# Kernel tuning notes

Hardware: AMD Instinct MI355X
Metric: run time of the kernel (lower is better)

Reference implementation:

```python
import jax, jax.numpy as jnp
import numpy as np

C = 201        # n_classes + 1 (background)
K = 5          # prototypes per class
DIM = 768
B = 64
HP = 16        # patch grid side, n_patches = HP*HP
N_PATCH = HP * HP
GAMMA = 0.999
SK_ITERS = 3
EPS = 1e-12


def setup_inputs() -> dict:
    key = jax.random.key(0)
    k1, k2, k3, k4 = jax.random.split(key, 4)
    return dict(
        patch_tokens=jax.random.normal(k1, (B, N_PATCH, DIM), jnp.float32),
        prototypes=jax.random.normal(k2, (C, K, DIM), jnp.float32) * 0.02,  # trunc_normal(std=0.02) approx
        sa=jnp.full((C - 1, K), 0.5, jnp.float32),                          # sa_init=0.5
        scale=jnp.float32(4.0),                                             # scale_init=4.0
        labels=jax.random.randint(k3, (B,), 0, C - 1),                      # image-level labels in [0, 200)
        masks=jax.random.bernoulli(k4, 0.5, (B, HP, HP)),                   # fg_extractor output
    )


def _masked_sinkhorn(L, m, n_iters=SK_ITERS):
    """Sinkhorn-Knopp over a masked subset of rows.
    L: [N, K] logits, m: [N] bool row mask. Rows outside m stay zero.
    Equivalent to running SK on the gathered rows L[m] (softmax init,
    alternating column/row normalization)."""
    Q = jax.nn.softmax(L, axis=-1) * m[:, None]

    def body(Q, _):
        Q = Q / (Q.sum(axis=0, keepdims=True) + EPS)                         # column normalize
        Q = jnp.where(m[:, None], Q / (Q.sum(axis=1, keepdims=True) + EPS), 0.0)  # row normalize (masked rows)
        return Q, None

    Q, _ = jax.lax.scan(body, Q, None, length=n_iters)
    return Q


def reference(patch_tokens, prototypes, sa, scale, labels, masks):
    # --- cosine patch-prototype logits ---
    tok = patch_tokens / (jnp.linalg.norm(patch_tokens, axis=-1, keepdims=True) + EPS)
    pro = prototypes / (jnp.linalg.norm(prototypes, axis=-1, keepdims=True) + EPS)
    patch_prototype_logits = jnp.einsum('bnd,ckd->bnck', tok, pro)           # [B, N, C, K]

    # --- avg pooling over patches ---
    image_prototype_logits = patch_prototype_logits.mean(axis=1)             # [B, C, K]

    # --- 'sa' classification head ---
    sa_w = jax.nn.softmax(sa, axis=-1) * K                                   # [C-1, K]
    class_logits = (scale * image_prototype_logits[:, :-1, :] * sa_w).sum(-1)  # [B, C-1]

    # --- pseudo patch labels from fg masks ---
    pseudo_patch_labels = jnp.where(masks, labels[:, None, None], C - 1)     # [B, H, W] int
    pl_flat = pseudo_patch_labels.reshape(-1)                                # [B*N]

    # --- online clustering (operates on detached values in the original) ---
    tok_flat = jax.lax.stop_gradient(tok).reshape(-1, DIM)                   # [B*N, D]
    L_flat = jax.lax.stop_gradient(patch_prototype_logits).reshape(-1, C, K)  # [B*N, C, K]
    class_mask = pl_flat[None, :] == jnp.arange(C)[:, None]                  # [C, B*N]

    # vectorized per-class masked Sinkhorn-Knopp (replaces dynamic python loop over unique labels)
    Q_all = jax.vmap(_masked_sinkhorn, in_axes=(1, 0))(L_flat, class_mask)   # [C, B*N, K]

    # prototype candidates: P_c_new = L_c_assignment^T @ I_c (masked rows are zero)
    P_new_c = jnp.einsum('cnk,nd->ckd', Q_all, tok_flat)                     # [C, K, D]
    has_class = class_mask.any(axis=1)[:, None, None]
    new_prototypes = jnp.where(has_class,
                               GAMMA * prototypes + (1.0 - GAMMA) * P_new_c,
                               prototypes)

    # part assignment: argmax over K, gathered at each patch's own class
    idx_all = jnp.argmax(Q_all, axis=-1)                                     # [C, B*N]
    part_assignment_maps = idx_all[pl_flat, jnp.arange(pl_flat.shape[0])].reshape(B, N_PATCH)

    return (patch_prototype_logits, image_prototype_logits, class_logits,
            part_assignment_maps, new_prototypes, pseudo_patch_labels)
```

## Files before the change

### kernel.cpp

```cpp
#include <hip/hip_runtime.h>
#include <hip/hip_cooperative_groups.h>
#include <math.h>

namespace cg = cooperative_groups;

#define NTOK 16384
#define NPRO 1005
#define DIMD 768
#define CKD  1005
#define CC   201
#define KKp  5
#define BGC  200
#define KEXP 2304
#define KA   1536
#define NPAD 1024

#define OUT_LOGITS   0
#define OUT_IMG      16465920
#define OUT_CLS      (OUT_IMG + 64320)
#define OUT_PART     (OUT_CLS + 12800)
#define OUT_NEWPROTO (OUT_PART + 16384)
#define OUT_PSEUDO   (OUT_NEWPROTO + 771840)

#define WOFF_PACC    0ULL
#define WOFF_COLSUM3 3087360ULL
#define WOFF_COUNTS  3099648ULL
#define WOFF_FLAG    3100672ULL
#define WS_ZERO_B    3100928ULL
#define WOFF_A2      3100928ULL
#define WOFF_B2      53432576ULL
#define WOFF_INVTOK  58151168ULL
#define WOFF_PL      58216704ULL
#define WOFF_Q       58282240ULL
#define WOFF_OFFSETS 58609920ULL
#define WOFF_CURSORS 58610944ULL
#define WOFF_ORDER   58611968ULL

typedef __attribute__((ext_vector_type(8))) short short8;
typedef __attribute__((ext_vector_type(4))) float f32x4;
typedef __attribute__((ext_vector_type(4))) unsigned short usv4;

__device__ __forceinline__ unsigned short f2bf(float x) {
  unsigned int b = __float_as_uint(x);
  unsigned int r = (b + 0x7FFFu + ((b >> 16) & 1u)) >> 16;
  return (unsigned short)r;
}
__device__ __forceinline__ float bf2f(unsigned short u) {
  return __uint_as_float(((unsigned int)u) << 16);
}

__device__ __forceinline__ void async_copy16(const void* g, void* lds) {
  __builtin_amdgcn_global_load_lds(
      (const __attribute__((address_space(1))) unsigned int*)g,
      (__attribute__((address_space(3))) unsigned int*)lds, 16, 0, 0);
}

__global__ __launch_bounds__(256) void conv_kernel(const float* __restrict__ tok,
                                                   const float* __restrict__ pro,
                                                   unsigned short* __restrict__ A2,
                                                   unsigned short* __restrict__ B2,
                                                   float* __restrict__ inv_tok) {
  int wid = (blockIdx.x * 256 + threadIdx.x) >> 6;
  int lane = threadIdx.x & 63;
  if (wid >= NTOK + NPAD) return;

  if (wid < NTOK) {
    const float4* s4 = (const float4*)(tok + (size_t)wid * DIMD);
    float4 v[3];
    float s = 0.0f;
#pragma unroll
    for (int p = 0; p < 3; ++p) {
      v[p] = s4[p * 64 + lane];
      s += v[p].x * v[p].x + v[p].y * v[p].y + v[p].z * v[p].z + v[p].w * v[p].w;
    }
#pragma unroll
    for (int off = 32; off; off >>= 1) s += __shfl_xor(s, off, 64);
    float inv = 1.0f / (sqrtf(s) + 1e-12f);
    if (lane == 0) inv_tok[wid] = inv;
    unsigned short* rowp = A2 + (size_t)wid * KA;
#pragma unroll
    for (int p = 0; p < 3; ++p) {
      float x0 = v[p].x * inv, x1 = v[p].y * inv, x2 = v[p].z * inv, x3 = v[p].w * inv;
      usv4 hi, lo;
      hi.x = f2bf(x0); hi.y = f2bf(x1); hi.z = f2bf(x2); hi.w = f2bf(x3);
      lo.x = f2bf(x0 - bf2f(hi.x)); lo.y = f2bf(x1 - bf2f(hi.y));
      lo.z = f2bf(x2 - bf2f(hi.z)); lo.w = f2bf(x3 - bf2f(hi.w));
      int c = p * 256 + lane * 4;
      *(usv4*)(rowp + c) = hi;
      *(usv4*)(rowp + 768 + c) = lo;
    }
  } else {
    int pw = wid - NTOK;
    unsigned short* rowp = B2 + (size_t)pw * KEXP;
    if (pw >= NPRO) {
      usv4 z = {0, 0, 0, 0};
#pragma unroll
      for (int p = 0; p < 3; ++p) {
        int c = p * 256 + lane * 4;
        *(usv4*)(rowp + c) = z; *(usv4*)(rowp + 768 + c) = z; *(usv4*)(rowp + 1536 + c) = z;
      }
      return;
    }
    const float4* s4 = (const float4*)(pro + (size_t)pw * DIMD);
    float4 v[3];
    float s = 0.0f;
#pragma unroll
    for (int p = 0; p < 3; ++p) {
      v[p] = s4[p * 64 + lane];
      s += v[p].x * v[p].x + v[p].y * v[p].y + v[p].z * v[p].z + v[p].w * v[p].w;
    }
#pragma unroll
    for (int off = 32; off; off >>= 1) s += __shfl_xor(s, off, 64);
    float inv = 1.0f / (sqrtf(s) + 1e-12f);
#pragma unroll
    for (int p = 0; p < 3; ++p) {
      float x0 = v[p].x * inv, x1 = v[p].y * inv, x2 = v[p].z * inv, x3 = v[p].w * inv;
      usv4 hi, lo;
      hi.x = f2bf(x0); hi.y = f2bf(x1); hi.z = f2bf(x2); hi.w = f2bf(x3);
      lo.x = f2bf(x0 - bf2f(hi.x)); lo.y = f2bf(x1 - bf2f(hi.y));
      lo.z = f2bf(x2 - bf2f(hi.z)); lo.w = f2bf(x3 - bf2f(hi.w));
      int c = p * 256 + lane * 4;
      *(usv4*)(rowp + c) = hi;
      *(usv4*)(rowp + 768 + c) = hi;
      *(usv4*)(rowp + 1536 + c) = lo;
    }
  }
}

__global__ __launch_bounds__(256, 2) void gemm_kernel(const unsigned short* __restrict__ A2,
                                                      const unsigned short* __restrict__ B2,
                                                      float* __restrict__ C,
                                                      float* __restrict__ img) {
  __shared__ unsigned short As[2][4096];
  __shared__ unsigned short Bs[2][4096];
  const int tid = threadIdx.x;
  const int lane = tid & 63, wave = tid >> 6;
  const int m0 = blockIdx.x * 128, n0 = blockIdx.y * 128;
  const int wr = wave >> 1, wc = wave & 1;

  f32x4 acc[4][4];
#pragma unroll
  for (int i = 0; i < 4; ++i)
#pragma unroll
    for (int j = 0; j < 4; ++j) acc[i][j] = (f32x4){0.f, 0.f, 0.f, 0.f};

  const int r4 = lane >> 2;
  const int kc = (lane & 3) * 8;

  auto STAGE = [&](int buf, int kt) {
    int kb = kt * 32;
    int acol = (kb < KA ? kb : kb - KA) + kc;
    int bcol = kb + kc;
#pragma unroll
    for (int j = 0; j < 2; ++j) {
      int seg = wave * 2 + j;
      async_copy16(A2 + (size_t)(m0 + seg * 16 + r4) * KA + acol, &As[buf][seg * 512]);
      async_copy16(B2 + (size_t)(n0 + seg * 16 + r4) * KEXP + bcol, &Bs[buf][seg * 512]);
    }
  };

  STAGE(0, 0);
  __syncthreads();

  const int rb = wr * 64 + (lane & 15);
  const int cb = wc * 64 + (lane & 15);
  const int hi8 = (lane >> 4) * 8;

  int cur = 0;
  for (int kt = 0; kt < 72; ++kt) {
    if (kt < 71) STAGE(cur ^ 1, kt + 1);
    short8 a[4], b[4];
#pragma unroll
    for (int ff = 0; ff < 4; ++ff) {
      a[ff] = *(const short8*)&As[cur][(rb + ff * 16) * 32 + hi8];
      b[ff] = *(const short8*)&Bs[cur][(cb + ff * 16) * 32 + hi8];
    }
#pragma unroll
    for (int fm = 0; fm < 4; ++fm)
#pragma unroll
      for (int fn = 0; fn < 4; ++fn)
        acc[fm][fn] = __builtin_amdgcn_mfma_f32_16x16x32_bf16(a[fm], b[fn], acc[fm][fn], 0, 0, 0);
    __syncthreads();
    cur ^= 1;
  }

  const int bimg = m0 >> 8;
#pragma unroll
  for (int fn = 0; fn < 4; ++fn) {
    int col = n0 + wc * 64 + fn * 16 + (lane & 15);
    float s = 0.0f;
#pragma unroll
    for (int fm = 0; fm < 4; ++fm) {
      int row = m0 + wr * 64 + fm * 16 + (lane >> 4) * 4;
      f32x4 v = acc[fm][fn];
      if (col < NPRO) {
        C[(size_t)(row + 0) * CKD + col] = v.x;
        C[(size_t)(row + 1) * CKD + col] = v.y;
        C[(size_t)(row + 2) * CKD + col] = v.z;
        C[(size_t)(row + 3) * CKD + col] = v.w;
      }
      s += v.x + v.y + v.z + v.w;
    }
    s += __shfl_xor(s, 16, 64);
    s += __shfl_xor(s, 32, 64);
    if (lane < 16 && col < NPRO)
      atomicAdd(&img[bimg * CKD + col], s * (1.0f / 256.0f));
  }
}

__global__ __launch_bounds__(256) void cls_kernel(const float* __restrict__ img,
                                                  const float* __restrict__ sa,
                                                  const float* __restrict__ scale,
                                                  float* __restrict__ out_cls) {
  int gid = blockIdx.x * 256 + threadIdx.x;
  if (gid >= 64 * 200) return;
  int b = gid / 200, c = gid - b * 200;
  float s5[KKp];
  float mx = -1e30f;
#pragma unroll
  for (int k = 0; k < KKp; ++k) { s5[k] = sa[c * KKp + k]; mx = fmaxf(mx, s5[k]); }
  float den = 0.0f;
#pragma unroll
  for (int k = 0; k < KKp; ++k) { s5[k] = expf(s5[k] - mx); den += s5[k]; }
  float acc = 0.0f;
#pragma unroll
  for (int k = 0; k < KKp; ++k)
    acc += img[(size_t)b * CKD + c * KKp + k] * (s5[k] / den * 5.0f);
  out_cls[gid] = scale[0] * acc;
}

__global__ __launch_bounds__(256) void cluster_kernel(const void* __restrict__ masks,
                                                      const int* __restrict__ labels,
                                                      const float* __restrict__ L,
                                                      float* __restrict__ Q,
                                                      int* __restrict__ pl,
                                                      float* __restrict__ out_pseudo,
                                                      float* __restrict__ out_part,
                                                      int* __restrict__ counts,
                                                      int* __restrict__ offsets,
                                                      int* __restrict__ cursors,
                                                      int* __restrict__ order,
                                                      float* __restrict__ colsum3,
                                                      int* __restrict__ flag) {
  cg::grid_group g = cg::this_grid();
  const int b = blockIdx.x, t = threadIdx.x;
  const int n = b * 256 + t;
  const int lane = t & 63, w = t >> 6;

  __shared__ int wcnt[4];
  __shared__ int sbase[2];
  __shared__ float red[4][2 * KKp];
  __shared__ int sc[256];

  if (t < 64) {
    unsigned v = ((const unsigned*)masks)[b * 64 + t];
    unsigned pr = (v == 0x3F800000u) ? 1u : (v > 1u ? 2u : 0u);
    if (pr) atomicOr(flag, (int)pr);
  }
  g.sync();
  int f = __hip_atomic_load(flag, __ATOMIC_RELAXED, __HIP_MEMORY_SCOPE_AGENT);

  int m;
  if (f & 1)      m = ((const float*)masks)[n] != 0.0f;
  else if (f & 2) m = ((const unsigned char*)masks)[n] != 0;
  else            m = ((const int*)masks)[n] != 0;
  const int cf = labels[b];
  const int lab = m ? cf : BGC;
  pl[n] = lab;
  out_pseudo[n] = (float)lab;

  unsigned long long mk = __ballot(m != 0);
  int rkw_fg = __popcll(mk & ((1ull << lane) - 1));
  int rkw_bg = lane - rkw_fg;
  if (lane == 0) wcnt[w] = __popcll(mk);
  __syncthreads();
  int fg_before = 0;
#pragma unroll
  for (int i = 0; i < 4; ++i) fg_before += (i < w) ? wcnt[i] : 0;
  int nf = wcnt[0] + wcnt[1] + wcnt[2] + wcnt[3];
  int fgrank = fg_before + rkw_fg;
  int bgrank = (w * 64 - fg_before) + rkw_bg;
  if (t == 0) {
    atomicAdd(&counts[cf], nf);
    atomicAdd(&counts[BGC], 256 - nf);
  }

  const float* Lr = L + (size_t)n * CKD + lab * KKp;
  float q[KKp];
  float mx = -1e30f;
#pragma unroll
  for (int k = 0; k < KKp; ++k) { q[k] = Lr[k]; mx = fmaxf(mx, q[k]); }
  float den = 0.0f;
#pragma unroll
  for (int k = 0; k < KKp; ++k) { q[k] = expf(q[k] - mx); den += q[k]; }
  float inv = 1.0f / den;
#pragma unroll
  for (int k = 0; k < KKp; ++k) q[k] *= inv;

  for (int it = 0; it < 3; ++it) {
    float fgv[KKp], bgv[KKp];
#pragma unroll
    for (int k = 0; k < KKp; ++k) { fgv[k] = m ? q[k] : 0.0f; bgv[k] = m ? 0.0f : q[k]; }
#pragma unroll
    for (int off = 32; off; off >>= 1) {
#pragma unroll
      for (int k = 0; k < KKp; ++k) {
        fgv[k] += __shfl_xor(fgv[k], off, 64);
        bgv[k] += __shfl_xor(bgv[k], off, 64);
      }
    }
    if (lane == 0) {
#pragma unroll
      for (int k = 0; k < KKp; ++k) { red[w][k] = fgv[k]; red[w][KKp + k] = bgv[k]; }
    }
    __syncthreads();
    if (t < 2 * KKp) {
      float s = red[0][t] + red[1][t] + red[2][t] + red[3][t];
      int cls_ = (t < KKp) ? cf : BGC;
      int kk = (t < KKp) ? t : t - KKp;
      atomicAdd(&colsum3[it * 1024 + cls_ * KKp + kk], s);
    }
    g.sync();

    if (it == 0 && b == 0) {
      int v0 = (t < CC) ? counts[t] : 0;
      sc[t] = v0;
      __syncthreads();
      for (int off = 1; off < 256; off <<= 1) {
        int u = (t >= off) ? sc[t - off] : 0;
        __syncthreads();
        sc[t] += u;
        __syncthreads();
      }
      if (t < CC) { offsets[t] = sc[t] - v0; cursors[t] = sc[t] - v0; }
      if (t == CC - 1) offsets[CC] = sc[t];
    }

    float r = 0.0f;
#pragma unroll
    for (int k = 0; k < KKp; ++k) {
      q[k] = q[k] / (colsum3[it * 1024 + lab * KKp + k] + 1e-12f);
      r += q[k];
    }
    float rinv = 1.0f / (r + 1e-12f);
#pragma unroll
    for (int k = 0; k < KKp; ++k) q[k] *= rinv;
  }

  float* Qr = Q + (size_t)n * KKp;
  float best = q[0];
  int bi = 0;
#pragma unroll
  for (int k = 0; k < KKp; ++k) {
    Qr[k] = q[k];
    if (k > 0 && q[k] > best) { best = q[k]; bi = k; }
  }
  out_part[n] = (float)bi;

  if (t == 0) {
    sbase[0] = atomicAdd(&cursors[cf], nf);
    sbase[1] = atomicAdd(&cursors[BGC], 256 - nf);
  }
  __syncthreads();
  int base = m ? sbase[0] : sbase[1];
  int rank = m ? fgrank : bgrank;
  order[base + rank] = n;
}

__global__ __launch_bounds__(256) void pnew_kernel(const int* __restrict__ order,
                                                   const int* __restrict__ pl,
                                                   const float* __restrict__ Q,
                                                   const float* __restrict__ tok,
                                                   const float* __restrict__ inv_tok,
                                                   float* __restrict__ P_acc) {
  __shared__ int idx[32], cls[32];
  int t = threadIdx.x;
  int p0 = blockIdx.x * 32;
  if (t < 32) {
    int n = order[p0 + t];
    idx[t] = n;
    cls[t] = pl[n];
  }
  __syncthreads();
  float acc[KKp][3];
#pragma unroll
  for (int k = 0; k < KKp; ++k)
#pragma unroll
    for (int s = 0; s < 3; ++s) acc[k][s] = 0.0f;
  int cur = cls[0];
  for (int i = 0; i < 32; ++i) {
    int c = cls[i];
    if (c != cur) {
#pragma unroll
      for (int k = 0; k < KKp; ++k)
#pragma unroll
        for (int s = 0; s < 3; ++s) {
          atomicAdd(&P_acc[((size_t)cur * KKp + k) * DIMD + s * 256 + t], acc[k][s]);
          acc[k][s] = 0.0f;
        }
      cur = c;
    }
    int n = idx[i];
    float it = inv_tok[n];
    float q[KKp];
#pragma unroll
    for (int k = 0; k < KKp; ++k) q[k] = Q[(size_t)n * KKp + k];
#pragma unroll
    for (int s = 0; s < 3; ++s) {
      float v = tok[(size_t)n * DIMD + s * 256 + t] * it;
#pragma unroll
      for (int k = 0; k < KKp; ++k) acc[k][s] = fmaf(q[k], v, acc[k][s]);
    }
  }
#pragma unroll
  for (int k = 0; k < KKp; ++k)
#pragma unroll
    for (int s = 0; s < 3; ++s)
      atomicAdd(&P_acc[((size_t)cur * KKp + k) * DIMD + s * 256 + t], acc[k][s]);
}

__global__ __launch_bounds__(256) void newproto_kernel(const float* __restrict__ proto,
                                                       const float* __restrict__ P_acc,
                                                       const int* __restrict__ offsets,
                                                       float* __restrict__ outp) {
  int gid = blockIdx.x * 256 + threadIdx.x;
  if (gid >= CC * KKp * DIMD) return;
  int c = gid / (KKp * DIMD);
  float p = proto[gid];
  bool has = offsets[c + 1] > offsets[c];
  outp[gid] = has ? (0.999f * p + 0.001f * P_acc[gid]) : p;
}

extern "C" void kernel_launch(void* const* d_in, const int* in_sizes, int n_in,
                              void* d_out, int out_size, void* d_ws, size_t ws_size,
                              hipStream_t stream) {
  const float* patch_tokens = (const float*)d_in[0];
  const float* prototypes   = (const float*)d_in[1];
  const float* sa           = (const float*)d_in[2];
  const float* scale        = (const float*)d_in[3];
  const int*   labels       = (const int*)d_in[4];
  const void*  masks        = (const void*)d_in[5];

  float* out = (float*)d_out;
  float* out_logits  = out + OUT_LOGITS;
  float* out_img     = out + OUT_IMG;
  float* out_cls     = out + OUT_CLS;
  float* out_part    = out + OUT_PART;
  float* out_newp    = out + OUT_NEWPROTO;
  float* out_pseudo  = out + OUT_PSEUDO;

  char* w = (char*)d_ws;
  float*          P_acc   = (float*)(w + WOFF_PACC);
  float*          colsum3 = (float*)(w + WOFF_COLSUM3);
  int*            counts  = (int*)(w + WOFF_COUNTS);
  int*            flag    = (int*)(w + WOFF_FLAG);
  unsigned short* A2      = (unsigned short*)(w + WOFF_A2);
  unsigned short* B2      = (unsigned short*)(w + WOFF_B2);
  float*          inv_tok = (float*)(w + WOFF_INVTOK);
  int*            pl      = (int*)(w + WOFF_PL);
  float*          Q       = (float*)(w + WOFF_Q);
  int*            offsets = (int*)(w + WOFF_OFFSETS);
  int*            cursors = (int*)(w + WOFF_CURSORS);
  int*            order   = (int*)(w + WOFF_ORDER);

  hipMemsetAsync(d_ws, 0, WS_ZERO_B, stream);
  hipMemsetAsync(out_img, 0, (size_t)64 * CKD * sizeof(float), stream);

  conv_kernel<<<4352, 256, 0, stream>>>(patch_tokens, prototypes, A2, B2, inv_tok);

  gemm_kernel<<<dim3(128, 8), 256, 0, stream>>>(A2, B2, out_logits, out_img);

  cls_kernel<<<50, 256, 0, stream>>>(out_img, sa, scale, out_cls);

  {
    const void* masks_a = masks; const int* labels_a = labels;
    const float* L_a = out_logits; float* Q_a = Q;
    int* pl_a = pl; float* pseudo_a = out_pseudo; float* part_a = out_part;
    int* counts_a = counts; int* offsets_a = offsets; int* cursors_a = cursors;
    int* order_a = order; float* colsum3_a = colsum3; int* flag_a = flag;
    void* cargs[] = {&masks_a, &labels_a, &L_a, &Q_a, &pl_a, &pseudo_a, &part_a,
                     &counts_a, &offsets_a, &cursors_a, &order_a, &colsum3_a, &flag_a};
    hipLaunchCooperativeKernel((const void*)cluster_kernel, dim3(64), dim3(256),
                               cargs, 0, stream);
  }

  pnew_kernel<<<512, 256, 0, stream>>>(order, pl, Q, patch_tokens, inv_tok, P_acc);
  newproto_kernel<<<3015, 256, 0, stream>>>(prototypes, P_acc, offsets, out_newp);
}
```

Before: 321.1 us.

## Enlarge GEMM tile to 256x256 with swizzled LDS pipeline; fold cls into cluster

The logits GEMM goes from a 128x128 tile with 4 waves to a 256x256 tile with 8 waves. It uses 128KB of dynamic LDS with a swizzled layout, K-steps of 64, and staged half-tile async loads interleaved with MFMA phases using barriers and setprio. The goal is more data reuse per block and less LDS bank conflict and global traffic. The separate cls_kernel is merged into the cooperative cluster_kernel, which removes one launch. The trade-off is higher register pressure and far fewer blocks (256 instead of 1024), which may hurt occupancy and load balance.

```diff
diff --git a/kernel.cpp b/kernel.cpp
--- a/kernel.cpp
+++ b/kernel.cpp
@@ -14,6 +14,7 @@
 #define KEXP 2304
 #define KA   1536
 #define NPAD 1024
+#define NT   36
 
 #define OUT_LOGITS   0
 #define OUT_IMG      16465920
@@ -127,71 +128,143 @@
   }
 }
 
-__global__ __launch_bounds__(256, 2) void gemm_kernel(const unsigned short* __restrict__ A2,
+__global__ __launch_bounds__(512, 2) void gemm_kernel(const unsigned short* __restrict__ A2,
                                                       const unsigned short* __restrict__ B2,
                                                       float* __restrict__ C,
                                                       float* __restrict__ img) {
-  __shared__ unsigned short As[2][4096];
-  __shared__ unsigned short Bs[2][4096];
+  extern __shared__ unsigned char lds[];
   const int tid = threadIdx.x;
-  const int lane = tid & 63, wave = tid >> 6;
-  const int m0 = blockIdx.x * 128, n0 = blockIdx.y * 128;
-  const int wr = wave >> 1, wc = wave & 1;
-
-  f32x4 acc[4][4];
-#pragma unroll
-  for (int i = 0; i < 4; ++i)
+  const int l = tid & 63, w = tid >> 6;
+  const int wr = w >> 2, wn = w & 3;
+  const int m0 = blockIdx.x * 256, n0 = blockIdx.y * 256;
+
+  f32x4 acc[8][4];
+#pragma unroll
+  for (int i = 0; i < 8; ++i)
 #pragma unroll
     for (int j = 0; j < 4; ++j) acc[i][j] = (f32x4){0.f, 0.f, 0.f, 0.f};
 
-  const int r4 = lane >> 2;
-  const int kc = (lane & 3) * 8;
-
-  auto STAGE = [&](int buf, int kt) {
-    int kb = kt * 32;
-    int acol = (kb < KA ? kb : kb - KA) + kc;
-    int bcol = kb + kc;
+  auto STAGE = [&](int t, int isB, int half) {
+    const int buf = t & 1;
+    unsigned char* dst = lds + (isB ? 65536 : 0) + buf * 32768 + half * 16384 + w * 1024;
+    const char* gsrc;
+    int rs;
+    if (isB) {
+      gsrc = (const char*)B2 + (size_t)(n0 + half * 128) * 4608 + (size_t)t * 128;
+      rs = 4608;
+    } else {
+      int ac = (t < 24 ? t : t - 24) * 128;
+      gsrc = (const char*)A2 + (size_t)(m0 + half * 128) * 3072 + ac;
+      rs = 3072;
+    }
 #pragma unroll
     for (int j = 0; j < 2; ++j) {
-      int seg = wave * 2 + j;
-      async_copy16(A2 + (size_t)(m0 + seg * 16 + r4) * KA + acol, &As[buf][seg * 512]);
-      async_copy16(B2 + (size_t)(n0 + seg * 16 + r4) * KEXP + bcol, &Bs[buf][seg * 512]);
+      int X = j * 8192 + w * 1024 + l * 16;
+      int P = X ^ (((X >> 8) & 1) << 4) ^ (((X >> 9) & 1) << 5);
+      int row = P >> 7, colb = P & 127;
+      async_copy16(gsrc + (size_t)row * rs + colb, dst + j * 8192);
     }
   };
 
-  STAGE(0, 0);
-  __syncthreads();
-
-  const int rb = wr * 64 + (lane & 15);
-  const int cb = wc * 64 + (lane & 15);
-  const int hi8 = (lane >> 4) * 8;
-
-  int cur = 0;
-  for (int kt = 0; kt < 72; ++kt) {
-    if (kt < 71) STAGE(cur ^ 1, kt + 1);
-    short8 a[4], b[4];
-#pragma unroll
-    for (int ff = 0; ff < 4; ++ff) {
-      a[ff] = *(const short8*)&As[cur][(rb + ff * 16) * 32 + hi8];
-      b[ff] = *(const short8*)&Bs[cur][(cb + ff * 16) * 32 + hi8];
-    }
+  STAGE(0, 0, 0); STAGE(0, 0, 1); STAGE(0, 1, 0); STAGE(0, 1, 1);
+  STAGE(1, 0, 0); STAGE(1, 0, 1);
+  asm volatile("s_waitcnt vmcnt(4)" ::: "memory");
+  __builtin_amdgcn_s_barrier();
+
+  const int lx = ((l >> 4) * 16) ^ ((l & 6) << 3);
+  const int arow = (l & 15) * 128 + lx;
+
+  short8 a0[4][2], a1[4][2], b0[2][2], b1[2][2];
+
+#pragma unroll 1
+  for (int t = 0; t < NT; ++t) {
+    const int buf = t & 1;
+    const unsigned char* ab = lds + buf * 32768 + wr * 16384;
+    const unsigned char* bb = lds + 65536 + buf * 32768 + (wn >> 1) * 16384 + (wn & 1) * 8192;
+
 #pragma unroll
     for (int fm = 0; fm < 4; ++fm)
 #pragma unroll
-      for (int fn = 0; fn < 4; ++fn)
-        acc[fm][fn] = __builtin_amdgcn_mfma_f32_16x16x32_bf16(a[fm], b[fn], acc[fm][fn], 0, 0, 0);
-    __syncthreads();
-    cur ^= 1;
+      for (int ks = 0; ks < 2; ++ks)
+        a0[fm][ks] = *(const short8*)(ab + fm * 2048 + ks * 64 + arow);
+#pragma unroll
+    for (int fn = 0; fn < 2; ++fn)
+#pragma unroll
+      for (int ks = 0; ks < 2; ++ks)
+        b0[fn][ks] = *(const short8*)(bb + fn * 2048 + ks * 64 + arow);
+    if (t + 1 < NT) STAGE(t + 1, 1, 0);
+    __builtin_amdgcn_s_barrier();
+    __builtin_amdgcn_s_setprio(1);
+#pragma unroll
+    for (int fm = 0; fm < 4; ++fm)
+#pragma unroll
+      for (int fn = 0; fn < 2; ++fn)
+#pragma unroll
+        for (int ks = 0; ks < 2; ++ks)
+          acc[fm][fn] = __builtin_amdgcn_mfma_f32_16x16x32_bf16(a0[fm][ks], b0[fn][ks], acc[fm][fn], 0, 0, 0);
+    __builtin_amdgcn_s_setprio(0);
+    __builtin_amdgcn_s_barrier();
+
+#pragma unroll
+    for (int fm = 0; fm < 4; ++fm)
+#pragma unroll
+      for (int ks = 0; ks < 2; ++ks)
+        a1[fm][ks] = *(const short8*)(ab + (4 + fm) * 2048 + ks * 64 + arow);
+    if (t + 1 < NT) STAGE(t + 1, 1, 1);
+    __builtin_amdgcn_s_barrier();
+    __builtin_amdgcn_s_setprio(1);
+#pragma unroll
+    for (int fm = 0; fm < 4; ++fm)
+#pragma unroll
+      for (int fn = 0; fn < 2; ++fn)
+#pragma unroll
+        for (int ks = 0; ks < 2; ++ks)
+          acc[4 + fm][fn] = __builtin_amdgcn_mfma_f32_16x16x32_bf16(a1[fm][ks], b0[fn][ks], acc[4 + fm][fn], 0, 0, 0);
+    __builtin_amdgcn_s_setprio(0);
+    __builtin_amdgcn_s_barrier();
+
+#pragma unroll
+    for (int fn = 0; fn < 2; ++fn)
+#pragma unroll
+      for (int ks = 0; ks < 2; ++ks)
+        b1[fn][ks] = *(const short8*)(bb + (2 + fn) * 2048 + ks * 64 + arow);
+    if (t + 2 < NT) STAGE(t + 2, 0, 0);
+    __builtin_amdgcn_s_barrier();
+    __builtin_amdgcn_s_setprio(1);
+#pragma unroll
+    for (int fm = 0; fm < 4; ++fm)
+#pragma unroll
+      for (int fn = 0; fn < 2; ++fn)
+#pragma unroll
+        for (int ks = 0; ks < 2; ++ks)
+          acc[fm][2 + fn] = __builtin_amdgcn_mfma_f32_16x16x32_bf16(a0[fm][ks], b1[fn][ks], acc[fm][2 + fn], 0, 0, 0);
+    __builtin_amdgcn_s_setprio(0);
+    __builtin_amdgcn_s_barrier();
+
+    if (t + 2 < NT) STAGE(t + 2, 0, 1);
+    __builtin_amdgcn_s_barrier();
+    __builtin_amdgcn_s_setprio(1);
+#pragma unroll
+    for (int fm = 0; fm < 4; ++fm)
+#pragma unroll
+      for (int fn = 0; fn < 2; ++fn)
+#pragma unroll
+        for (int ks = 0; ks < 2; ++ks)
+          acc[4 + fm][2 + fn] = __builtin_amdgcn_mfma_f32_16x16x32_bf16(a1[fm][ks], b1[fn][ks], acc[4 + fm][2 + fn], 0, 0, 0);
+    __builtin_amdgcn_s_setprio(0);
+    if (t < NT - 2) asm volatile("s_waitcnt vmcnt(4)" ::: "memory");
+    else if (t == NT - 2) asm volatile("s_waitcnt vmcnt(0)" ::: "memory");
+    __builtin_amdgcn_s_barrier();
   }
 
   const int bimg = m0 >> 8;
 #pragma unroll
   for (int fn = 0; fn < 4; ++fn) {
-    int col = n0 + wc * 64 + fn * 16 + (lane & 15);
+    int col = n0 + wn * 64 + fn * 16 + (l & 15);
     float s = 0.0f;
 #pragma unroll
-    for (int fm = 0; fm < 4; ++fm) {
-      int row = m0 + wr * 64 + fm * 16 + (lane >> 4) * 4;
+    for (int fm = 0; fm < 8; ++fm) {
+      int row = m0 + wr * 128 + fm * 16 + (l >> 4) * 4;
       f32x4 v = acc[fm][fn];
       if (col < NPRO) {
         C[(size_t)(row + 0) * CKD + col] = v.x;
@@ -203,35 +276,18 @@
     }
     s += __shfl_xor(s, 16, 64);
     s += __shfl_xor(s, 32, 64);
-    if (lane < 16 && col < NPRO)
+    if (l < 16 && col < NPRO)
       atomicAdd(&img[bimg * CKD + col], s * (1.0f / 256.0f));
   }
-}
-
-__global__ __launch_bounds__(256) void cls_kernel(const float* __restrict__ img,
-                                                  const float* __restrict__ sa,
-                                                  const float* __restrict__ scale,
-                                                  float* __restrict__ out_cls) {
-  int gid = blockIdx.x * 256 + threadIdx.x;
-  if (gid >= 64 * 200) return;
-  int b = gid / 200, c = gid - b * 200;
-  float s5[KKp];
-  float mx = -1e30f;
-#pragma unroll
-  for (int k = 0; k < KKp; ++k) { s5[k] = sa[c * KKp + k]; mx = fmaxf(mx, s5[k]); }
-  float den = 0.0f;
-#pragma unroll
-  for (int k = 0; k < KKp; ++k) { s5[k] = expf(s5[k] - mx); den += s5[k]; }
-  float acc = 0.0f;
-#pragma unroll
-  for (int k = 0; k < KKp; ++k)
-    acc += img[(size_t)b * CKD + c * KKp + k] * (s5[k] / den * 5.0f);
-  out_cls[gid] = scale[0] * acc;
 }
 
 __global__ __launch_bounds__(256) void cluster_kernel(const void* __restrict__ masks,
                                                       const int* __restrict__ labels,
                                                       const float* __restrict__ L,
+                                                      const float* __restrict__ img,
+                                                      const float* __restrict__ sa,
+                                                      const float* __restrict__ scale,
+                                                      float* __restrict__ out_cls,
                                                       float* __restrict__ Q,
                                                       int* __restrict__ pl,
                                                       float* __restrict__ out_pseudo,
@@ -252,6 +308,21 @@
   __shared__ float red[4][2 * KKp];
   __shared__ int sc[256];
 
+  if (t < 200) {
+    float s5[KKp];
+    float mx = -1e30f;
+#pragma unroll
+    for (int k = 0; k < KKp; ++k) { s5[k] = sa[t * KKp + k]; mx = fmaxf(mx, s5[k]); }
+    float den = 0.0f;
+#pragma unroll
+    for (int k = 0; k < KKp; ++k) { s5[k] = expf(s5[k] - mx); den += s5[k]; }
+    float a = 0.0f;
+#pragma unroll
+    for (int k = 0; k < KKp; ++k)
+      a += img[(size_t)b * CKD + t * KKp + k] * (s5[k] / den * 5.0f);
+    out_cls[b * 200 + t] = scale[0] * a;
+  }
+
   if (t < 64) {
     unsigned v = ((const unsigned*)masks)[b * 64 + t];
     unsigned pr = (v == 0x3F800000u) ? 1u : (v > 1u ? 2u : 0u);
@@ -463,22 +534,26 @@
   int*            cursors = (int*)(w + WOFF_CURSORS);
   int*            order   = (int*)(w + WOFF_ORDER);
 
+  hipFuncSetAttribute((const void*)gemm_kernel,
+                      hipFuncAttributeMaxDynamicSharedMemorySize, 131072);
+
   hipMemsetAsync(d_ws, 0, WS_ZERO_B, stream);
   hipMemsetAsync(out_img, 0, (size_t)64 * CKD * sizeof(float), stream);
 
   conv_kernel<<<4352, 256, 0, stream>>>(patch_tokens, prototypes, A2, B2, inv_tok);
 
-  gemm_kernel<<<dim3(128, 8), 256, 0, stream>>>(A2, B2, out_logits, out_img);
-
-  cls_kernel<<<50, 256, 0, stream>>>(out_img, sa, scale, out_cls);
+  gemm_kernel<<<dim3(64, 4), 512, 131072, stream>>>(A2, B2, out_logits, out_img);
 
   {
     const void* masks_a = masks; const int* labels_a = labels;
-    const float* L_a = out_logits; float* Q_a = Q;
+    const float* L_a = out_logits; const float* img_a = out_img;
+    const float* sa_a = sa; const float* scale_a = scale; float* cls_a = out_cls;
+    float* Q_a = Q;
     int* pl_a = pl; float* pseudo_a = out_pseudo; float* part_a = out_part;
     int* counts_a = counts; int* offsets_a = offsets; int* cursors_a = cursors;
     int* order_a = order; float* colsum3_a = colsum3; int* flag_a = flag;
-    void* cargs[] = {&masks_a, &labels_a, &L_a, &Q_a, &pl_a, &pseudo_a, &part_a,
+    void* cargs[] = {&masks_a, &labels_a, &L_a, &img_a, &sa_a, &scale_a, &cls_a,
+                     &Q_a, &pl_a, &pseudo_a, &part_a,
                      &counts_a, &offsets_a, &cursors_a, &order_a, &colsum3_a, &flag_a};
     hipLaunchCooperativeKernel((const void*)cluster_kernel, dim3(64), dim3(256),
                                cargs, 0, stream);
```

New measurement: 313.5 us. -2.4%, faster.
